# Kernel tuning notes

Measured on AMD Instinct MI355X. Metric: run time of the kernel, lower is better.

Reference implementation:

```python
import jax, jax.numpy as jnp
import numpy as np

ALPHA, GAMMA = 0.25, 2.0
LOC_CW, CLS_CW, OBJ_CW = 1.0, 0.25, 0.1
LOC_W, CLS_W, OBJ_W = 1.0, 1.0, 1.0
B, K, N, C, D = 128, 2048, 4, 64, 3


def _lsa_rows(cost):
    """Hungarian (Kuhn-Munkres with potentials). cost: [n,m], n<=m.
    Returns col assigned to each row (same optimum as scipy.linear_sum_assignment)."""
    cost = np.asarray(cost, dtype=np.float64)
    n, m = cost.shape
    u = np.zeros(n + 1); v = np.zeros(m + 1)
    p = np.zeros(m + 1, dtype=np.int64)
    way = np.zeros(m + 1, dtype=np.int64)
    for i in range(1, n + 1):
        p[0] = i; j0 = 0
        minv = np.full(m + 1, np.inf)
        used = np.zeros(m + 1, dtype=bool)
        while True:
            used[j0] = True
            i0 = p[j0]
            cur = cost[i0 - 1] - u[i0] - v[1:]
            mv = minv[1:]; wy = way[1:]
            free = ~used[1:]
            upd = free & (cur < mv)
            mv[upd] = cur[upd]; wy[upd] = j0
            jrel = np.where(free)[0]
            j1 = jrel[np.argmin(mv[jrel])] + 1
            delta = mv[j1 - 1]
            uj = np.where(used)[0]
            u[p[uj]] += delta
            v[uj] -= delta
            mv[free] -= delta
            j0 = j1
            if p[j0] == 0:
                break
        while j0:
            j1 = way[j0]; p[j0] = p[j1]; j0 = j1
    col_of_row = np.full(n, -1, dtype=np.int64)
    for j in range(1, m + 1):
        if p[j] > 0:
            col_of_row[p[j] - 1] = j - 1
    return col_of_row


def focal_bce(logits, targets, alpha=ALPHA, gamma=GAMMA):
    p = jax.nn.sigmoid(logits)
    # stable BCE-with-logits
    ce = jnp.maximum(logits, 0.0) - logits * targets + jnp.log1p(jnp.exp(-jnp.abs(logits)))
    p_t = p * targets + (1.0 - p) * (1.0 - targets)
    alpha_t = alpha * targets + (1.0 - alpha) * (1.0 - targets)
    return alpha_t * ce * (1.0 - p_t) ** gamma


def _match(loc_out, obj_logit, cls_logit, gt_loc, gt_cls):
    """Hungarian matching (detached, matches torch no_grad block). Returns pred_idx [B,N];
    gt index n is matched to prediction pred_idx[b,n]."""
    eps = 1e-8
    vp = loc_out / jnp.clip(jnp.linalg.norm(loc_out, axis=-1, keepdims=True), eps)
    vt = gt_loc / jnp.clip(jnp.linalg.norm(gt_loc, axis=-1, keepdims=True), eps)
    cos = jnp.clip(jnp.einsum('bkd,bnd->bkn', vp, vt), -1.0 + 1e-6, 1.0 - 1e-6)
    loc_cost = jnp.arccos(cos) / jnp.pi  # [B,K,N]
    # cls cost: focal BCE summed over POSITIVE classes only / pos_count.
    # focal(x, t=1) = alpha * softplus(-x) * (1 - sigmoid(x))**gamma  -> einsum with one-hot gts
    focal_pos = ALPHA * jax.nn.softplus(-cls_logit) * (1.0 - jax.nn.sigmoid(cls_logit)) ** GAMMA  # [B,K,C]
    pos_cnt = jnp.maximum(gt_cls.sum(-1), 1.0)  # [B,N]
    cls_cost = jnp.einsum('bkc,bnc->bkn', focal_pos, gt_cls) / pos_cnt[:, None, :]
    obj_cost = -jax.nn.sigmoid(obj_logit)[:, :, None]  # [B,K,1]
    total = LOC_CW * loc_cost + CLS_CW * cls_cost + OBJ_CW * obj_cost  # [B,K,N]
    total_np = np.asarray(jax.device_get(total))
    # transpose to [N,K] so rows (gt) <= cols (preds)
    pred_idx = np.stack([_lsa_rows(total_np[b].T) for b in range(total_np.shape[0])])
    return jnp.asarray(pred_idx)  # [B,N] int


def _losses(loc_out, obj_logit, cls_logit, gt_loc, gt_cls, pred_idx):
    b, k = loc_out.shape[0], loc_out.shape[1]
    mp_loc = jnp.take_along_axis(loc_out, pred_idx[:, :, None], axis=1)  # [B,N,D]
    mp_cls = jnp.take_along_axis(cls_logit, pred_idx[:, :, None], axis=1)  # [B,N,C]
    # loc criterion = MSE; per-sample mean then /B == global mean (all samples have N>0)
    loc_loss = jnp.mean((mp_loc - gt_loc) ** 2)
    cls_loss = jnp.mean(focal_bce(mp_cls, gt_cls))
    obj_target = jnp.zeros((b, k), dtype=obj_logit.dtype).at[jnp.arange(b)[:, None], pred_idx].set(1.0)
    obj_ce = jnp.maximum(obj_logit, 0.0) - obj_logit * obj_target + jnp.log1p(jnp.exp(-jnp.abs(obj_logit)))
    obj_loss = jnp.mean(obj_ce)
    return LOC_W * loc_loss + CLS_W * cls_loss + OBJ_W * obj_loss


def setup_inputs() -> dict:
    key = jax.random.key(0)
    k1, k2, k3, k4, k5 = jax.random.split(key, 5)
    loc_out = jax.random.normal(k1, (B, K, D), dtype=jnp.float32)
    obj_logit = jax.random.normal(k2, (B, K), dtype=jnp.float32)
    cls_logit = jax.random.normal(k3, (B, K, C), dtype=jnp.float32)
    gt_loc = jax.random.normal(k4, (B, N, D), dtype=jnp.float32)
    cls_idx = jax.random.randint(k5, (B, N), 0, C)
    gt_cls = jax.nn.one_hot(cls_idx, C, dtype=jnp.float32)
    return {'loc_out': loc_out, 'obj_logit': obj_logit, 'cls_logit': cls_logit,
            'gt_loc': gt_loc, 'gt_cls': gt_cls}


def reference(loc_out, obj_logit, cls_logit, gt_loc, gt_cls):
    pred_idx = _match(loc_out, obj_logit, cls_logit, gt_loc, gt_cls)
    return _losses(loc_out, obj_logit, cls_logit, gt_loc, gt_cls, pred_idx)
```

## Files before the change

kernel.cpp:

```cpp
#include <hip/hip_runtime.h>
#include <math.h>
#include <limits.h>

#define BB 128
#define KK 2048
#define NN 4
#define CC 64
#define DD 3
#define SL 8
#define KS (KK/SL)
#define THREADS 256

#define OFF_CVAL 0
#define OFF_CIDX (BB*SL*NN*NN)
#define OFF_OBJ  (2*BB*SL*NN*NN)

__device__ __forceinline__ float acospi_fast(float x) {
    float ax = fabsf(x);
    float p = ((-0.0187293f*ax + 0.0742610f)*ax - 0.2121144f)*ax + 1.5707288f;
    float r = sqrtf(1.f - ax) * p;
    r = (x >= 0.f) ? r : 3.14159274f - r;
    return r * 0.31830988618379067f;
}

__global__ void __launch_bounds__(THREADS)
crit_cost(const float* __restrict__ loc_out, const float* __restrict__ obj_logit,
          const float* __restrict__ cls_logit, const float* __restrict__ gt_loc,
          const float* __restrict__ gt_cls, float* __restrict__ ws,
          float* __restrict__ out)
{
    __shared__ float cost[NN][KS];
    __shared__ float obj_s[4];

    const int sl  = blockIdx.x;
    const int b   = blockIdx.y;
    const int tid = threadIdx.x;
    const int w   = tid >> 6, lane = tid & 63;
    const int k   = sl*KS + tid;

    if (sl == 0 && b == 0 && tid == 0) out[0] = 0.f;

    const float* lp = loc_out + ((size_t)b*KK + k)*DD;
    float l0 = lp[0], l1 = lp[1], l2 = lp[2];
    float x  = obj_logit[b*KK + k];

    int   cls[NN]; float posin[NN];
    #pragma unroll
    for (int n = 0; n < NN; ++n) {
        float v = gt_cls[(b*NN+n)*CC + lane];
        unsigned long long m = __ballot(v > 0.5f);
        cls[n]   = __ffsll(m) - 1;
        posin[n] = 1.f / fmaxf((float)__popcll(m), 1.f);
    }

    float z[NN];
    #pragma unroll
    for (int n = 0; n < NN; ++n)
        z[n] = cls_logit[((size_t)b*KK + k)*CC + cls[n]];

    float vt[NN][DD];
    #pragma unroll
    for (int n = 0; n < NN; ++n) {
        float g0 = gt_loc[(b*NN+n)*DD+0];
        float g1 = gt_loc[(b*NN+n)*DD+1];
        float g2 = gt_loc[(b*NN+n)*DD+2];
        float gin = 1.f / fmaxf(sqrtf(g0*g0 + g1*g1 + g2*g2), 1e-8f);
        vt[n][0] = g0*gin; vt[n][1] = g1*gin; vt[n][2] = g2*gin;
    }

    float inv = 1.f / fmaxf(sqrtf(l0*l0 + l1*l1 + l2*l2), 1e-8f);
    float v0 = l0*inv, v1 = l1*inv, v2 = l2*inv;
    float obj_base = fmaxf(x, 0.f) + log1pf(expf(-fabsf(x)));
    float oc = -0.1f / (1.f + __expf(-x));
    #pragma unroll
    for (int n = 0; n < NN; ++n) {
        float cosv = v0*vt[n][0] + v1*vt[n][1] + v2*vt[n][2];
        cosv = fminf(fmaxf(cosv, -1.f + 1e-6f), 1.f - 1e-6f);
        float loc_c = acospi_fast(cosv);
        float zz = z[n];
        float e  = __expf(-fabsf(zz));
        float lg = __logf(1.f + e);
        float sp = (zz >= 0.f) ? lg : (lg - zz);
        float r1 = 1.f / (1.f + e);
        float sn = (zz >= 0.f) ? e*r1 : r1;
        float fp = 0.25f * sp * sn * sn;
        cost[n][tid] = loc_c + 0.25f*fp*posin[n] + oc;
    }

    float osum = obj_base;
    #pragma unroll
    for (int off = 32; off > 0; off >>= 1) osum += __shfl_xor(osum, off, 64);
    if (lane == 0) obj_s[w] = osum;
    __syncthreads();

    float vv[4]; int gi[4];
    #pragma unroll
    for (int j = 0; j < 4; ++j) {
        vv[j] = cost[w][lane + 64*j];
        gi[j] = sl*KS + lane + 64*j;
    }
    float cr_val[NN]; int cr_idx[NN];
    #pragma unroll
    for (int r = 0; r < NN; ++r) {
        float bv = vv[0]; int bi = gi[0];
        #pragma unroll
        for (int j = 1; j < 4; ++j)
            if (vv[j] < bv || (vv[j] == bv && gi[j] < bi)) { bv = vv[j]; bi = gi[j]; }
        #pragma unroll
        for (int off = 32; off > 0; off >>= 1) {
            float ov = __shfl_xor(bv, off, 64);
            int   oi = __shfl_xor(bi, off, 64);
            if (ov < bv || (ov == bv && oi < bi)) { bv = ov; bi = oi; }
        }
        cr_val[r] = bv; cr_idx[r] = bi;
        #pragma unroll
        for (int j = 0; j < 4; ++j) if (gi[j] == bi) vv[j] = INFINITY;
    }
    if (lane == 0) {
        int base = ((b*SL + sl)*NN + w)*NN;
        int* wsi = (int*)ws;
        #pragma unroll
        for (int r = 0; r < NN; ++r) {
            ws[OFF_CVAL + base + r]  = cr_val[r];
            wsi[OFF_CIDX + base + r] = cr_idx[r];
        }
    }
    if (tid == 0)
        ws[OFF_OBJ + b*SL + sl] = obj_s[0] + obj_s[1] + obj_s[2] + obj_s[3];
}

__global__ void __launch_bounds__(THREADS)
crit_match(const float* __restrict__ loc_out, const float* __restrict__ obj_logit,
           const float* __restrict__ cls_logit, const float* __restrict__ gt_loc,
           const float* __restrict__ gt_cls, float* __restrict__ ws,
           float* __restrict__ out)
{
    __shared__ float cand_val[NN][NN];
    __shared__ int   cand_idx[NN][NN];
    __shared__ int   s_pred[NN];
    __shared__ float s_best[4];
    __shared__ int   s_bestc[4];
    __shared__ float red[4];
    __shared__ float s_lo;

    const int b = blockIdx.x, tid = threadIdx.x;
    const int w = tid >> 6, lane = tid & 63;
    const int* wsi = (const int*)ws;

    {
        float v = INFINITY; int idx = INT_MAX;
        if (lane < SL*NN) {
            int sl = lane >> 2, r = lane & 3;
            int base = ((b*SL + sl)*NN + w)*NN + r;
            v   = ws[OFF_CVAL + base];
            idx = wsi[OFF_CIDX + base];
        }
        #pragma unroll
        for (int r = 0; r < NN; ++r) {
            float bv = v; int bi = idx;
            #pragma unroll
            for (int off = 32; off > 0; off >>= 1) {
                float ov = __shfl_xor(bv, off, 64);
                int   oi = __shfl_xor(bi, off, 64);
                if (ov < bv || (ov == bv && oi < bi)) { bv = ov; bi = oi; }
            }
            if (lane == 0) { cand_val[w][r] = bv; cand_idx[w][r] = bi; }
            if (idx == bi) v = INFINITY;
        }
    }
    __syncthreads();

    {
        int a0 = (tid >> 6) & 3, a1 = (tid >> 4) & 3, a2 = (tid >> 2) & 3, a3 = tid & 3;
        int c0 = cand_idx[0][a0], c1 = cand_idx[1][a1];
        int c2 = cand_idx[2][a2], c3 = cand_idx[3][a3];
        bool valid = (c0!=c1) & (c0!=c2) & (c0!=c3) & (c1!=c2) & (c1!=c3) & (c2!=c3);
        float t = cand_val[0][a0] + cand_val[1][a1] + cand_val[2][a2] + cand_val[3][a3];
        float bv = valid ? t : INFINITY;
        int   bc = tid;
        #pragma unroll
        for (int off = 32; off > 0; off >>= 1) {
            float ov = __shfl_xor(bv, off, 64);
            int   oc = __shfl_xor(bc, off, 64);
            if (ov < bv || (ov == bv && oc < bc)) { bv = ov; bc = oc; }
        }
        if (lane == 0) { s_best[w] = bv; s_bestc[w] = bc; }
    }
    __syncthreads();

    if (tid == 0) {
        float bv = s_best[0]; int bc = s_bestc[0];
        for (int i = 1; i < 4; ++i)
            if (s_best[i] < bv || (s_best[i] == bv && s_bestc[i] < bc)) { bv = s_best[i]; bc = s_bestc[i]; }
        int a0 = (bc >> 6) & 3, a1 = (bc >> 4) & 3, a2 = (bc >> 2) & 3, a3 = bc & 3;
        s_pred[0] = cand_idx[0][a0]; s_pred[1] = cand_idx[1][a1];
        s_pred[2] = cand_idx[2][a2]; s_pred[3] = cand_idx[3][a3];

        float om = 0.f;
        for (int sl = 0; sl < SL; ++sl) om += ws[OFF_OBJ + b*SL + sl];
        for (int n = 0; n < NN; ++n) om -= obj_logit[b*KK + s_pred[n]];

        float s = 0.f;
        for (int n = 0; n < NN; ++n)
            for (int d = 0; d < DD; ++d) {
                float diff = loc_out[((size_t)b*KK + s_pred[n])*DD + d] - gt_loc[(b*NN+n)*DD + d];
                s += diff*diff;
            }
        s_lo = s / (float)(BB*NN*DD) + om / (float)(BB*KK);
    }
    __syncthreads();

    {
        int n = w, c = lane;
        float zz = cls_logit[((size_t)b*KK + s_pred[n])*CC + c];
        float tgt = gt_cls[(b*NN+n)*CC + c];
        float p  = 1.f / (1.f + expf(-zz));
        float ce = fmaxf(zz, 0.f) - zz*tgt + log1pf(expf(-fabsf(zz)));
        float pt = p*tgt + (1.f-p)*(1.f-tgt);
        float at = 0.25f*tgt + 0.75f*(1.f-tgt);
        float om1 = 1.f - pt;
        float r = at * ce * om1 * om1;
        #pragma unroll
        for (int off = 32; off > 0; off >>= 1) r += __shfl_xor(r, off, 64);
        if (lane == 0) red[n] = r;
    }
    __syncthreads();

    if (tid == 0) {
        float total = s_lo + (red[0] + red[1] + red[2] + red[3]) / (float)(BB*NN*CC);
        atomicAdd(out, total);
    }
}

extern "C" void kernel_launch(void* const* d_in, const int* in_sizes, int n_in,
                              void* d_out, int out_size, void* d_ws, size_t ws_size,
                              hipStream_t stream) {
    const float* loc_out   = (const float*)d_in[0];
    const float* obj_logit = (const float*)d_in[1];
    const float* cls_logit = (const float*)d_in[2];
    const float* gt_loc    = (const float*)d_in[3];
    const float* gt_cls    = (const float*)d_in[4];
    float* ws  = (float*)d_ws;
    float* out = (float*)d_out;

    hipLaunchKernelGGL(crit_cost, dim3(SL, BB), dim3(THREADS), 0, stream,
                       loc_out, obj_logit, cls_logit, gt_loc, gt_cls, ws, out);
    hipLaunchKernelGGL(crit_match, dim3(BB), dim3(THREADS), 0, stream,
                       loc_out, obj_logit, cls_logit, gt_loc, gt_cls, ws, out);
}
```

Before: 27.80 us.

## Stage cls_logit slices into LDS with coalesced float4 loads, use smaller blocks

Instead of each thread gathering four scattered class logits from its own row, each block now loads its whole contiguous cls_logit slice into padded shared memory using float4 loads. It then reads the needed columns from LDS. The block is halved to 128 threads and SL is doubled to 16, so the top-4 reduction runs two rows per wave and crit_match's per-wave candidate read now fills all 64 lanes. This trades scattered uncoalesced global gathers for fully coalesced streaming, at the cost of about 33KB of LDS per block, which may limit occupancy.

```diff
diff --git a/kernel.cpp b/kernel.cpp
--- a/kernel.cpp
+++ b/kernel.cpp
@@ -7,9 +7,11 @@
 #define NN 4
 #define CC 64
 #define DD 3
-#define SL 8
+#define SL 16
 #define KS (KK/SL)
+#define TCOST 128
 #define THREADS 256
+#define LROW 65
 
 #define OFF_CVAL 0
 #define OFF_CIDX (BB*SL*NN*NN)
@@ -23,14 +25,15 @@
     return r * 0.31830988618379067f;
 }
 
-__global__ void __launch_bounds__(THREADS)
+__global__ void __launch_bounds__(TCOST)
 crit_cost(const float* __restrict__ loc_out, const float* __restrict__ obj_logit,
           const float* __restrict__ cls_logit, const float* __restrict__ gt_loc,
           const float* __restrict__ gt_cls, float* __restrict__ ws,
           float* __restrict__ out)
 {
+    __shared__ float zl[KS*LROW];
     __shared__ float cost[NN][KS];
-    __shared__ float obj_s[4];
+    __shared__ float obj_s[2];
 
     const int sl  = blockIdx.x;
     const int b   = blockIdx.y;
@@ -44,6 +47,19 @@
     float l0 = lp[0], l1 = lp[1], l2 = lp[2];
     float x  = obj_logit[b*KK + k];
 
+    {
+        const float4* zsrc = (const float4*)(cls_logit + (size_t)b*KK*CC + (size_t)sl*KS*CC);
+        #pragma unroll
+        for (int i = 0; i < (KS*CC/4)/TCOST; ++i) {
+            int f   = tid + TCOST*i;
+            float4 v = zsrc[f];
+            int row = f >> 4;
+            int c0  = (f & 15) << 2;
+            float* d = &zl[row*LROW + c0];
+            d[0] = v.x; d[1] = v.y; d[2] = v.z; d[3] = v.w;
+        }
+    }
+
     int   cls[NN]; float posin[NN];
     #pragma unroll
     for (int n = 0; n < NN; ++n) {
@@ -52,11 +68,6 @@
         cls[n]   = __ffsll(m) - 1;
         posin[n] = 1.f / fmaxf((float)__popcll(m), 1.f);
     }
-
-    float z[NN];
-    #pragma unroll
-    for (int n = 0; n < NN; ++n)
-        z[n] = cls_logit[((size_t)b*KK + k)*CC + cls[n]];
 
     float vt[NN][DD];
     #pragma unroll
@@ -72,12 +83,20 @@
     float v0 = l0*inv, v1 = l1*inv, v2 = l2*inv;
     float obj_base = fmaxf(x, 0.f) + log1pf(expf(-fabsf(x)));
     float oc = -0.1f / (1.f + __expf(-x));
+
+    float osum = obj_base;
+    #pragma unroll
+    for (int off = 32; off > 0; off >>= 1) osum += __shfl_xor(osum, off, 64);
+    if (lane == 0) obj_s[w] = osum;
+
+    __syncthreads();
+
     #pragma unroll
     for (int n = 0; n < NN; ++n) {
         float cosv = v0*vt[n][0] + v1*vt[n][1] + v2*vt[n][2];
         cosv = fminf(fmaxf(cosv, -1.f + 1e-6f), 1.f - 1e-6f);
         float loc_c = acospi_fast(cosv);
-        float zz = z[n];
+        float zz = zl[tid*LROW + cls[n]];
         float e  = __expf(-fabsf(zz));
         float lg = __logf(1.f + e);
         float sp = (zz >= 0.f) ? lg : (lg - zz);
@@ -86,47 +105,42 @@
         float fp = 0.25f * sp * sn * sn;
         cost[n][tid] = loc_c + 0.25f*fp*posin[n] + oc;
     }
-
-    float osum = obj_base;
-    #pragma unroll
-    for (int off = 32; off > 0; off >>= 1) osum += __shfl_xor(osum, off, 64);
-    if (lane == 0) obj_s[w] = osum;
-    __syncthreads();
-
-    float vv[4]; int gi[4];
-    #pragma unroll
-    for (int j = 0; j < 4; ++j) {
-        vv[j] = cost[w][lane + 64*j];
-        gi[j] = sl*KS + lane + 64*j;
-    }
-    float cr_val[NN]; int cr_idx[NN];
-    #pragma unroll
-    for (int r = 0; r < NN; ++r) {
-        float bv = vv[0]; int bi = gi[0];
-        #pragma unroll
-        for (int j = 1; j < 4; ++j)
-            if (vv[j] < bv || (vv[j] == bv && gi[j] < bi)) { bv = vv[j]; bi = gi[j]; }
-        #pragma unroll
-        for (int off = 32; off > 0; off >>= 1) {
-            float ov = __shfl_xor(bv, off, 64);
-            int   oi = __shfl_xor(bi, off, 64);
-            if (ov < bv || (ov == bv && oi < bi)) { bv = ov; bi = oi; }
-        }
-        cr_val[r] = bv; cr_idx[r] = bi;
-        #pragma unroll
-        for (int j = 0; j < 4; ++j) if (gi[j] == bi) vv[j] = INFINITY;
-    }
-    if (lane == 0) {
-        int base = ((b*SL + sl)*NN + w)*NN;
-        int* wsi = (int*)ws;
-        #pragma unroll
-        for (int r = 0; r < NN; ++r) {
-            ws[OFF_CVAL + base + r]  = cr_val[r];
-            wsi[OFF_CIDX + base + r] = cr_idx[r];
+    __syncthreads();
+
+    int* wsi = (int*)ws;
+    for (int rr = w; rr < NN; rr += 2) {
+        float vv[2]; int gi[2];
+        #pragma unroll
+        for (int j = 0; j < 2; ++j) {
+            vv[j] = cost[rr][lane + 64*j];
+            gi[j] = sl*KS + lane + 64*j;
+        }
+        float cr_val[NN]; int cr_idx[NN];
+        #pragma unroll
+        for (int r = 0; r < 4; ++r) {
+            float bv = vv[0]; int bi = gi[0];
+            if (vv[1] < bv || (vv[1] == bv && gi[1] < bi)) { bv = vv[1]; bi = gi[1]; }
+            #pragma unroll
+            for (int off = 32; off > 0; off >>= 1) {
+                float ov = __shfl_xor(bv, off, 64);
+                int   oi = __shfl_xor(bi, off, 64);
+                if (ov < bv || (ov == bv && oi < bi)) { bv = ov; bi = oi; }
+            }
+            cr_val[r] = bv; cr_idx[r] = bi;
+            if (gi[0] == bi) vv[0] = INFINITY;
+            if (gi[1] == bi) vv[1] = INFINITY;
+        }
+        if (lane == 0) {
+            int base = ((b*SL + sl)*NN + rr)*NN;
+            #pragma unroll
+            for (int r = 0; r < NN; ++r) {
+                ws[OFF_CVAL + base + r]  = cr_val[r];
+                wsi[OFF_CIDX + base + r] = cr_idx[r];
+            }
         }
     }
     if (tid == 0)
-        ws[OFF_OBJ + b*SL + sl] = obj_s[0] + obj_s[1] + obj_s[2] + obj_s[3];
+        ws[OFF_OBJ + b*SL + sl] = obj_s[0] + obj_s[1];
 }
 
 __global__ void __launch_bounds__(THREADS)
@@ -148,15 +162,12 @@
     const int* wsi = (const int*)ws;
 
     {
-        float v = INFINITY; int idx = INT_MAX;
-        if (lane < SL*NN) {
-            int sl = lane >> 2, r = lane & 3;
-            int base = ((b*SL + sl)*NN + w)*NN + r;
-            v   = ws[OFF_CVAL + base];
-            idx = wsi[OFF_CIDX + base];
-        }
-        #pragma unroll
-        for (int r = 0; r < NN; ++r) {
+        int sl = lane >> 2, r = lane & 3;
+        int base = ((b*SL + sl)*NN + w)*NN + r;
+        float v = ws[OFF_CVAL + base];
+        int idx = wsi[OFF_CIDX + base];
+        #pragma unroll
+        for (int r2 = 0; r2 < NN; ++r2) {
             float bv = v; int bi = idx;
             #pragma unroll
             for (int off = 32; off > 0; off >>= 1) {
@@ -164,7 +175,7 @@
                 int   oi = __shfl_xor(bi, off, 64);
                 if (ov < bv || (ov == bv && oi < bi)) { bv = ov; bi = oi; }
             }
-            if (lane == 0) { cand_val[w][r] = bv; cand_idx[w][r] = bi; }
+            if (lane == 0) { cand_val[w][r2] = bv; cand_idx[w][r2] = bi; }
             if (idx == bi) v = INFINITY;
         }
     }
@@ -243,7 +254,7 @@
     float* ws  = (float*)d_ws;
     float* out = (float*)d_out;
 
-    hipLaunchKernelGGL(crit_cost, dim3(SL, BB), dim3(THREADS), 0, stream,
+    hipLaunchKernelGGL(crit_cost, dim3(SL, BB), dim3(TCOST), 0, stream,
                        loc_out, obj_logit, cls_logit, gt_loc, gt_cls, ws, out);
     hipLaunchKernelGGL(crit_match, dim3(BB), dim3(THREADS), 0, stream,
                        loc_out, obj_logit, cls_logit, gt_loc, gt_cls, ws, out);
```

New measurement: 38.90 us. 39.9% more time.
